# Performance work log

Hardware: AMD Instinct MI355X
Metric: run time of the kernel (lower is better)

Reference implementation:

```python
import jax, jax.numpy as jnp
import numpy as np
from jax import lax

sg = lax.stop_gradient

# (kernel, stride, pad, pool_k, pool_s) for the 7 conv blocks
CFG = [(16, 2, 7, 8, 4), (12, 2, 5, 4, 2), (9, 1, 4, 5, 2), (7, 1, 3, 4, 2),
       (5, 1, 2, 2, 2), (3, 1, 1, 2, 2), (3, 1, 1, 2, 2)]
W_SHAPES = [(8, 1, 16), (12, 8, 12), (32, 12, 9), (64, 32, 7),
            (64, 64, 5), (64, 64, 3), (72, 64, 3)]
CH = [8, 12, 32, 64, 64, 64, 72]


def bin_act(x):
    # forward: sign(x); backward: clipped-quadratic surrogate (STE)
    s = jnp.sign(x)
    le = (x < -1.0).astype(x.dtype)
    ri = (x >= 1.0).astype(x.dtype)
    cl = ((x >= -1.0) & (x < 0.0)).astype(x.dtype)
    cr = ((x >= 0.0) & (x < 1.0)).astype(x.dtype)
    out = cl * (2.0 + x) * x + cr * (2.0 - x) * x + ri - le
    return sg(s) + out - sg(out)


def bin_wei(w, axes):
    # forward: scale * sign(w) with scale = mean|w| (detached); backward through tanh (STE)
    scale = sg(jnp.mean(jnp.abs(w), axis=axes, keepdims=True))
    t = jnp.tanh(w)
    return sg(scale * jnp.sign(w)) + t - sg(t)


def conv1d(x, w, stride, pad):
    return lax.conv_general_dilated(x, w, (stride,), [(pad, pad)],
                                    dimension_numbers=('NCH', 'OIH', 'NCH'))


def maxpool1d(x, k, s):
    return lax.reduce_window(x, -jnp.inf, lax.max, (1, 1, k), (1, 1, s), 'VALID')


def batchnorm1d(x, gamma, beta, eps=1e-5):
    # training-mode BN: batch statistics over (N, L), biased variance
    m = jnp.mean(x, axis=(0, 2), keepdims=True)
    v = jnp.mean((x - m) ** 2, axis=(0, 2), keepdims=True)
    return gamma[None, :, None] * (x - m) / jnp.sqrt(v + eps) + beta[None, :, None]


def _forward(x, ws, gs, bs, wfc):
    for w, g, b, (k, s, p, pk, ps) in zip(ws, gs, bs, CFG):
        x = conv1d(x, bin_wei(w, (1, 2)), s, p)
        x = maxpool1d(x, pk, ps)
        x = batchnorm1d(x, g, b)
        x = bin_act(x)
    x = x.reshape(x.shape[0], -1)                 # [B, 72*3]
    return x @ bin_wei(wfc, (1,)).T               # [B, classCount]


def setup_inputs() -> dict:
    key = jax.random.key(0)
    ks = jax.random.split(key, 9)
    inp = {'x': jax.random.normal(ks[0], (2048, 1, 3600), dtype=jnp.float32)}
    for i, shp in enumerate(W_SHAPES):
        inp[f'w{i+1}'] = jax.random.uniform(ks[i + 1], shp, dtype=jnp.float32) * 0.32
        inp[f'g{i+1}'] = jnp.ones((CH[i],), jnp.float32)
        inp[f'b{i+1}'] = jnp.zeros((CH[i],), jnp.float32)
    inp['wfc'] = jax.random.uniform(ks[8], (5, 216), dtype=jnp.float32) * 0.32
    return inp


def reference(x, w1, w2, w3, w4, w5, w6, w7,
              g1, g2, g3, g4, g5, g6, g7,
              b1, b2, b3, b4, b5, b6, b7, wfc):
    ws = [w1, w2, w3, w4, w5, w6, w7]
    gs = [g1, g2, g3, g4, g5, g6, g7]
    bs = [b1, b2, b3, b4, b5, b6, b7]
    return _forward(x, ws, gs, bs, wfc)
```

## Files before the change

kernel.cpp:

```cpp
#include <hip/hip_runtime.h>
#include <math.h>
#include <stdint.h>

#define NBATCH 2048
#define NSLOT 32

struct Args {
    const float* x;
    const float* W[7];
    const float* G[7];
    const float* Bt[7];
    const float* WFC;
    float* out;
    float* bufA;
    float* bufB;
    double* stats;
    float* wsc;
    uint32_t* wmb;
};

__device__ __forceinline__ float signf(float v) {
    return (v > 0.f) ? 1.f : ((v < 0.f) ? -1.f : 0.f);
}

__global__ __launch_bounds__(256) void k_setup(Args a) {
    const int blk = blockIdx.x, tid = threadIdx.x;
    for (int i = blk * 256 + tid; i < NSLOT * 632; i += 391 * 256) a.stats[i] = 0.0;

    if (blk < 321 && tid < 64) {
        const int cum[9] = {0,8,20,52,116,180,244,316,321};
        const int per[8] = {16,96,108,224,320,192,192,216};
        const float* wsrc[8] = {a.W[0],a.W[1],a.W[2],a.W[3],a.W[4],a.W[5],a.W[6],a.WFC};
        int o = blk, L = 0;
        while (L < 7 && o >= cum[L + 1]) ++L;
        const int oo = o - cum[L], p = per[L];
        const float* wo = wsrc[L] + (size_t)oo * p;
        float s = 0.f;
        for (int i = tid; i < p; i += 64) s += fabsf(wo[i]);
        #pragma unroll
        for (int off = 32; off; off >>= 1) s += __shfl_down(s, off);
        if (tid == 0) a.wsc[o] = s / (float)p;
    }

    const int gid = (blk - 384) * 256 + tid;
    if (blk >= 384 && gid >= 0 && gid < 1608) {
        const int cum[7]  = {0,144,432,880,1200,1392,1608};
        const int cin[6]  = {8,12,32,64,64,64};
        const int kk[6]   = {12,9,7,5,3,3};
        const int wpp[6]  = {1,1,1,2,2,2};
        const int woff[6] = {0,144,432,880,1520,1904};
        const float* wsrc[6] = {a.W[1],a.W[2],a.W[3],a.W[4],a.W[5],a.W[6]};
        int L = 0;
        while (L < 5 && gid >= cum[L + 1]) ++L;
        const int idx = gid - cum[L];
        const int K = kk[L], CIN = cin[L], WPP = wpp[L];
        const int o = idx / K, k = idx - o * K;
        const float* w = wsrc[L];
        uint32_t m0 = 0, m1 = 0;
        for (int c = 0; c < CIN; ++c) {
            const float v = w[((size_t)o * CIN + c) * K + k];
            const uint32_t bit = (v < 0.f) ? 1u : 0u;
            int bp = c;
            if (CIN == 64) bp = 16 * (c & 3) + (c >> 2);
            else if (CIN == 32) bp = 8 * (c & 3) + (c >> 2);
            if (bp < 32) m0 |= bit << bp; else m1 |= bit << (bp - 32);
        }
        uint32_t* dst = a.wmb + woff[L] + (size_t)idx * WPP;
        dst[0] = m0;
        if (WPP == 2) dst[1] = m1;
    }
}

__global__ __launch_bounds__(256) void k_conv1(Args a) {
    __shared__ float wgs[128];
    __shared__ double sred[16];
    const int n = blockIdx.x, tid = threadIdx.x, l = tid & 63;
    if (tid < 128) wgs[tid] = signf(a.W[0][tid]);
    if (tid < 16)  sred[tid] = 0.0;
    __syncthreads();
    const int r = tid;
    const float* xn = a.x + (size_t)n * 3600;
    float m0[8], m1[8];
    #pragma unroll
    for (int ch = 0; ch < 8; ++ch) { m0[ch] = 0.f; m1[ch] = 0.f; }
    if (r < 225) {
        float f[40];
        const int g0 = 16 * r - 8;
        #pragma unroll
        for (int b = 0; b < 10; ++b) {
            const int gg = g0 + 4 * b;
            if (gg >= 0 && gg <= 3596) {
                const float4 v = *(const float4*)(xn + gg);
                f[4*b] = v.x; f[4*b+1] = v.y; f[4*b+2] = v.z; f[4*b+3] = v.w;
            } else {
                f[4*b] = 0.f; f[4*b+1] = 0.f; f[4*b+2] = 0.f; f[4*b+3] = 0.f;
            }
        }
        #pragma unroll
        for (int ch = 0; ch < 8; ++ch) {
            float acc[12];
            #pragma unroll
            for (int j = 0; j < 12; ++j) acc[j] = 0.f;
            #pragma unroll
            for (int k = 0; k < 16; ++k) {
                const float wk = wgs[ch * 16 + k];
                #pragma unroll
                for (int j = 0; j < 12; ++j)
                    acc[j] = fmaf(f[2*j + 1 + k], wk, acc[j]);
            }
            const float lo  = fmaxf(fmaxf(acc[0], acc[1]), fmaxf(acc[2], acc[3]));
            const float mid = fmaxf(fmaxf(acc[4], acc[5]), fmaxf(acc[6], acc[7]));
            const float hi  = fmaxf(fmaxf(acc[8], acc[9]), fmaxf(acc[10], acc[11]));
            const float sc = a.wsc[ch];
            m0[ch] = fmaxf(lo, mid) * sc;
            m1[ch] = (r < 224) ? fmaxf(mid, hi) * sc : 0.f;
        }
        float* on = a.bufA + ((size_t)n * 449 + 2 * r) * 8;
        *(float4*)(on + 0) = make_float4(m0[0], m0[1], m0[2], m0[3]);
        *(float4*)(on + 4) = make_float4(m0[4], m0[5], m0[6], m0[7]);
        if (r < 224) {
            *(float4*)(on + 8)  = make_float4(m1[0], m1[1], m1[2], m1[3]);
            *(float4*)(on + 12) = make_float4(m1[4], m1[5], m1[6], m1[7]);
        }
    }
    #pragma unroll
    for (int ch = 0; ch < 8; ++ch) {
        double sS = (double)m0[ch] + (double)m1[ch];
        double s2 = (double)m0[ch] * m0[ch] + (double)m1[ch] * m1[ch];
        #pragma unroll
        for (int off = 32; off; off >>= 1) {
            sS += __shfl_down(sS, off);
            s2 += __shfl_down(s2, off);
        }
        if (l == 0) {
            atomicAdd(&sred[ch], sS);
            atomicAdd(&sred[8 + ch], s2);
        }
    }
    __syncthreads();
    if (tid < 16) {
        double* so = a.stats + (size_t)(n & (NSLOT - 1)) * 16;
        atomicAdd(&so[tid], sred[tid]);
    }
}

template <int CIN, int LIN, int O, int K, int STRIDE, int PAD,
          int PK, int PS, int LP, int WPP, int LPB, bool SF64>
__device__ __forceinline__ void bin_body(
    const float* __restrict__ xprev, const uint32_t* __restrict__ wm,
    const float* __restrict__ wsc, const float* __restrict__ wsc_prev,
    const double* __restrict__ stats_in,
    const float* __restrict__ gamma, const float* __restrict__ beta,
    const double cntInv, float* __restrict__ out, double* __restrict__ stats_out)
{
    constexpr int OL    = (O < 64) ? O : 64;
    constexpr int PO    = 64 / OL;
    constexpr int SPAN  = (PK - 1) * STRIDE + K;
    constexpr int SHIFT = (WPP == 1) ? (PAD & 1) : 0;
    constexpr int QSPAN = 4 * LPB * PS * STRIDE + SPAN + 2;
    constexpr int XM64A = (WPP == 2) ? QSPAN : ((QSPAN + 3) / 2 + 1);
    constexpr int F     = 2 * CIN;
    constexpr int FW    = (F > 64) ? 128 : 64;

    __shared__ uint64_t xmbuf[XM64A];
    __shared__ long long foldU[4][FW];
    __shared__ int sS[4][O], sS2[4][O];

    const int tid = threadIdx.x;
    const int wv  = tid >> 6;
    const int l   = tid & 63;
    uint32_t* xm32 = (uint32_t*)xmbuf;
    uint64_t* xm64 = xmbuf;

    const int n    = blockIdx.x;
    const int lp0b = blockIdx.y * (4 * LPB);
    const int lp1b = (lp0b + 4 * LPB < LP) ? lp0b + 4 * LPB : LP;
    const int q0raw = lp0b * PS * STRIDE - PAD;
    const int q0 = (q0raw > 0) ? q0raw : 0;
    const int q1raw = (lp1b - 1) * PS * STRIDE - PAD + SPAN;
    const int q1 = (q1raw < LIN) ? q1raw : LIN;
    const int S0 = (WPP == 1) ? ((q0 + SHIFT) & 1) : 0;
    const int xbase = q0 - S0;

    const int lp0 = lp0b + wv * LPB;
    const int lp1 = (lp0 + LPB < lp1b) ? lp0 + LPB : lp1b;

    const float* xn = xprev + (size_t)n * LIN * CIN;

    {
        const long long* stI = (const long long*)stats_in;
        long long pa = 0, pb_ = 0;
        double da = 0.0;
        #pragma unroll
        for (int s8 = 0; s8 < 8; ++s8) {
            const int s = (wv << 3) + s8;
            if constexpr (SF64) {
                if (l < F) da += stats_in[s * F + l];
            } else {
                if (l < ((F < 64) ? F : 64)) pa += stI[s * F + l];
                if constexpr (F > 64) { if (l < F - 64) pb_ += stI[s * F + 64 + l]; }
            }
        }
        if constexpr (SF64) foldU[wv][l] = __double_as_longlong(da);
        else {
            foldU[wv][l] = pa;
            if constexpr (F > 64) foldU[wv][64 + l] = pb_;
        }
    }
    __syncthreads();
    float aA = 0.f, aB = 0.f;
    {
        double t0 = 0.0, t1 = 0.0;
        if constexpr (SF64) {
            double tot = 0.0;
            #pragma unroll
            for (int w = 0; w < 4; ++w) tot += __longlong_as_double(foldU[w][l]);
            t0 = tot;
            t1 = __shfl(tot, CIN + l);
        } else if constexpr (F > 64) {
            long long a0 = 0, a1 = 0;
            #pragma unroll
            for (int w = 0; w < 4; ++w) { a0 += foldU[w][l]; a1 += foldU[w][64 + l]; }
            t0 = (double)a0; t1 = (double)a1;
        } else {
            long long a0 = 0;
            #pragma unroll
            for (int w = 0; w < 4; ++w) a0 += foldU[w][l];
            const double tot = (double)a0;
            t0 = tot;
            t1 = __shfl(tot, CIN + l);
        }
        if (l < CIN) {
            double mean, E2;
            if constexpr (SF64) { mean = t0 * cntInv; E2 = t1 * cntInv; }
            else {
                const double w = (double)wsc_prev[l];
                mean = w * t0 * cntInv; E2 = w * w * t1 * cntInv;
            }
            const double var = E2 - mean * mean;
            const double inv = 1.0 / sqrt(var + 1e-5);
            const double av  = (double)gamma[l] * inv;
            aA = (float)av;
            aB = (float)((double)beta[l] - mean * av);
        }
    }

    if constexpr (CIN == 64) {
        const int sub = l & 15, grp = l >> 4;
        const float a0 = __shfl(aA, 4*sub),     b0 = __shfl(aB, 4*sub);
        const float a1 = __shfl(aA, 4*sub + 1), b1 = __shfl(aB, 4*sub + 1);
        const float a2 = __shfl(aA, 4*sub + 2), b2 = __shfl(aB, 4*sub + 2);
        const float a3 = __shfl(aA, 4*sub + 3), b3 = __shfl(aB, 4*sub + 3);
        for (int pb = q0 + wv * 4; pb < q1; pb += 16) {
            const int pos = pb + grp;
            const bool valid = pos < q1;
            const float4 v = *(const float4*)(xn + (size_t)(valid ? pos : q0) * 64 + 4*sub);
            const unsigned long long bal0 = __ballot(valid && (fmaf(a0, v.x, b0) < 0.f));
            const unsigned long long bal1 = __ballot(valid && (fmaf(a1, v.y, b1) < 0.f));
            const unsigned long long bal2 = __ballot(valid && (fmaf(a2, v.z, b2) < 0.f));
            const unsigned long long bal3 = __ballot(valid && (fmaf(a3, v.w, b3) < 0.f));
            if (l < 4 && pb + l < q1) {
                const uint64_t m = ((bal0 >> (16*l)) & 0xFFFFull)
                                 | (((bal1 >> (16*l)) & 0xFFFFull) << 16)
                                 | (((bal2 >> (16*l)) & 0xFFFFull) << 32)
                                 | (((bal3 >> (16*l)) & 0xFFFFull) << 48);
                xm64[pb + l - xbase] = m;
            }
        }
    } else if constexpr (CIN == 32) {
        const int sub = l & 7, grp = l >> 3;
        const float a0 = __shfl(aA, 4*sub),     b0 = __shfl(aB, 4*sub);
        const float a1 = __shfl(aA, 4*sub + 1), b1 = __shfl(aB, 4*sub + 1);
        const float a2 = __shfl(aA, 4*sub + 2), b2 = __shfl(aB, 4*sub + 2);
        const float a3 = __shfl(aA, 4*sub + 3), b3 = __shfl(aB, 4*sub + 3);
        for (int pb = q0 + wv * 8; pb < q1; pb += 32) {
            const int pos = pb + grp;
            const bool valid = pos < q1;
            const float4 v = *(const float4*)(xn + (size_t)(valid ? pos : q0) * 32 + 4*sub);
            const unsigned long long bal0 = __ballot(valid && (fmaf(a0, v.x, b0) < 0.f));
            const unsigned long long bal1 = __ballot(valid && (fmaf(a1, v.y, b1) < 0.f));
            const unsigned long long bal2 = __ballot(valid && (fmaf(a2, v.z, b2) < 0.f));
            const unsigned long long bal3 = __ballot(valid && (fmaf(a3, v.w, b3) < 0.f));
            if (l < 8 && pb + l < q1) {
                const uint32_t m = (uint32_t)((bal0 >> (8*l)) & 0xFFull)
                                 | ((uint32_t)((bal1 >> (8*l)) & 0xFFull) << 8)
                                 | ((uint32_t)((bal2 >> (8*l)) & 0xFFull) << 16)
                                 | ((uint32_t)((bal3 >> (8*l)) & 0xFFull) << 24);
                xm32[pb + l - xbase] = m;
            }
        }
    } else if constexpr (CIN == 8) {
        const int sub = l & 1, grp = l >> 1;
        const float a0 = __shfl(aA, 4*sub),     b0 = __shfl(aB, 4*sub);
        const float a1 = __shfl(aA, 4*sub + 1), b1 = __shfl(aB, 4*sub + 1);
        const float a2 = __shfl(aA, 4*sub + 2), b2 = __shfl(aB, 4*sub + 2);
        const float a3 = __shfl(aA, 4*sub + 3), b3 = __shfl(aB, 4*sub + 3);
        for (int pb = q0 + wv * 32; pb < q1; pb += 128) {
            const int pos = pb + grp;
            const bool valid = pos < q1;
            const float4 v = *(const float4*)(xn + (size_t)(valid ? pos : q0) * 8 + 4*sub);
            const unsigned long long bal0 = __ballot(valid && (fmaf(a0, v.x, b0) < 0.f));
            const unsigned long long bal1 = __ballot(valid && (fmaf(a1, v.y, b1) < 0.f));
            const unsigned long long bal2 = __ballot(valid && (fmaf(a2, v.z, b2) < 0.f));
            const unsigned long long bal3 = __ballot(valid && (fmaf(a3, v.w, b3) < 0.f));
            if (l < 32 && pb + l < q1) {
                const uint32_t t0 = (uint32_t)((bal0 >> (2*l)) & 3ull);
                const uint32_t t1 = (uint32_t)((bal1 >> (2*l)) & 3ull);
                const uint32_t t2 = (uint32_t)((bal2 >> (2*l)) & 3ull);
                const uint32_t t3 = (uint32_t)((bal3 >> (2*l)) & 3ull);
                const uint32_t m = (t0 & 1) | ((t1 & 1) << 1) | ((t2 & 1) << 2) | ((t3 & 1) << 3)
                                 | ((t0 >> 1) << 4) | ((t1 >> 1) << 5) | ((t2 >> 1) << 6) | ((t3 >> 1) << 7);
                xm32[pb + l - xbase] = m;
            }
        }
    } else {
        constexpr int PPW = 64 / CIN;
        const int pw = l / CIN, c = l - pw * CIN;
        const float myA = __shfl(aA, c), myB = __shfl(aB, c);
        const bool lact = (pw < PPW);
        for (int pb = q0 + wv * PPW; pb < q1; pb += 4 * PPW) {
            const int pos = pb + pw;
            const bool act = lact && (pos < q1);
            float v = 0.f;
            if (act) v = fmaf(myA, xn[(size_t)pb * CIN + l], myB);
            const unsigned long long bal = __ballot(act && (v < 0.f));
            if (act && c == 0) {
                const uint32_t mk = (uint32_t)((bal >> (pw * CIN)) & ((1u << CIN) - 1));
                xm32[pos - xbase] = mk;
            }
        }
    }
    __syncthreads();

    float* on = out + (size_t)n * LP * O;

    if constexpr (WPP == 2) {
        const uint64_t* wmp = (const uint64_t*)wm;
        uint64_t wr[K];
        #pragma unroll
        for (int k = 0; k < K; ++k) wr[k] = wmp[l * K + k];
        uint64_t wr2[K];
        const int oo2 = 64 + ((O > 64 && l < O - 64) ? l : 0);
        if constexpr (O > 64) {
            #pragma unroll
            for (int k = 0; k < K; ++k) wr2[k] = wmp[oo2 * K + k];
        }
        const float myws  = wsc[l];
        const float myws2 = (O > 64 && l < O - 64) ? wsc[64 + l] : 0.f;
        int accS = 0, accS2 = 0, accSb = 0, accS2b = 0;

        for (int lp = lp0; lp < lp1; ++lp) {
            const int lo = lp * PS * STRIDE - PAD;
            int m = -1000000, m2 = -1000000;
            if (lo >= 0 && lo + SPAN <= LIN) {
                uint64_t tw[SPAN];
                #pragma unroll
                for (int t = 0; t < SPAN; ++t) tw[t] = xm64[lo - xbase + t];
                #pragma unroll
                for (int j = 0; j < PK; ++j) {
                    int p = 0;
                    #pragma unroll
                    for (int k = 0; k < K; ++k)
                        p += __popcll(tw[j * STRIDE + k] ^ wr[k]);
                    m = max(m, CIN * K - 2 * p);
                    if constexpr (O > 64) {
                        int p2 = 0;
                        #pragma unroll
                        for (int k = 0; k < K; ++k)
                            p2 += __popcll(tw[j * STRIDE + k] ^ wr2[k]);
                        m2 = max(m2, CIN * K - 2 * p2);
                    }
                }
            } else {
                #pragma unroll
                for (int j = 0; j < PK; ++j) {
                    const int base = lo + j * STRIDE;
                    int p = 0, nv = 0, p2 = 0;
                    #pragma unroll
                    for (int k = 0; k < K; ++k) {
                        const int q = base + k;
                        if (q >= 0 && q < LIN) {
                            ++nv;
                            const uint64_t xv = xm64[q - xbase];
                            p += __popcll(xv ^ wr[k]);
                            if constexpr (O > 64) p2 += __popcll(xv ^ wr2[k]);
                        }
                    }
                    m = max(m, CIN * nv - 2 * p);
                    if constexpr (O > 64) m2 = max(m2, CIN * nv - 2 * p2);
                }
            }
            on[lp * O + l] = (float)m * myws;
            accS += m; accS2 += m * m;
            if constexpr (O > 64) {
                if (l < O - 64) {
                    on[lp * O + 64 + l] = (float)m2 * myws2;
                    accSb += m2; accS2b += m2 * m2;
                }
            }
        }
        sS[wv][l] = accS; sS2[wv][l] = accS2;
        if constexpr (O > 64) {
            if (l < O - 64) { sS[wv][64 + l] = accSb; sS2[wv][64 + l] = accS2b; }
        }
    } else {
        const int po = l / OL, oo = l - po * OL;
        const bool cact = (po < PO);
        const float myws = cact ? wsc[oo] : 0.f;
        uint32_t wr[K];
        #pragma unroll
        for (int k = 0; k < K; ++k) wr[k] = wm[(cact ? oo : 0) * K + k];
        int accS = 0, accS2 = 0;

        constexpr int PAIRS = (SPAN + 1) / 2;
        for (int lp = lp0 + po; lp < lp1; lp += PO) {
            const int lo = lp * PS * STRIDE - PAD;
            int m = -1000000;
            if (lo >= 0 && lo + SPAN <= LIN) {
                uint32_t tw[PAIRS * 2];
                const int e0 = (lo - xbase) >> 1;
                #pragma unroll
                for (int i = 0; i < PAIRS; ++i) {
                    const uint64_t u = xm64[e0 + i];
                    tw[2 * i]     = (uint32_t)u;
                    tw[2 * i + 1] = (uint32_t)(u >> 32);
                }
                #pragma unroll
                for (int j = 0; j < PK; ++j) {
                    int p = 0;
                    #pragma unroll
                    for (int k = 0; k < K; ++k)
                        p += __popc(tw[j * STRIDE + k] ^ wr[k]);
                    m = max(m, CIN * K - 2 * p);
                }
            } else {
                #pragma unroll
                for (int j = 0; j < PK; ++j) {
                    const int base = lo + j * STRIDE;
                    int p = 0, nv = 0;
                    #pragma unroll
                    for (int k = 0; k < K; ++k) {
                        const int q = base + k;
                        if (q >= 0 && q < LIN) { ++nv; p += __popc(xm32[q - xbase] ^ wr[k]); }
                    }
                    m = max(m, CIN * nv - 2 * p);
                }
            }
            if (cact) {
                on[lp * O + oo] = (float)m * myws;
                accS += m; accS2 += m * m;
            }
        }
        int t = accS, t2 = accS2;
        #pragma unroll
        for (int g = 1; g < PO; ++g) {
            t  += __shfl(accS,  l + g * OL);
            t2 += __shfl(accS2, l + g * OL);
        }
        if (l < OL) { sS[wv][l] = t; sS2[wv][l] = t2; }
    }
    __syncthreads();

    unsigned long long* soU =
        (unsigned long long*)stats_out + (size_t)(n & (NSLOT - 1)) * 2 * O;
    for (int t = tid; t < 2 * O; t += 256) {
        int tot;
        if (t < O) tot = sS[0][t] + sS[1][t] + sS[2][t] + sS[3][t];
        else { const int f = t - O; tot = sS2[0][f] + sS2[1][f] + sS2[2][f] + sS2[3][f]; }
        atomicAdd(&soU[t], (unsigned long long)(long long)tot);
    }
}

#define BIN_PARAMS \
    const float* __restrict__ xprev, const uint32_t* __restrict__ wm, \
    const float* __restrict__ wsc, const float* __restrict__ wsc_prev, \
    const double* __restrict__ stats_in, \
    const float* __restrict__ gamma, const float* __restrict__ beta, \
    const double cntInv, float* __restrict__ out, double* __restrict__ stats_out
#define BIN_ARGS xprev, wm, wsc, wsc_prev, stats_in, gamma, beta, cntInv, out, stats_out

__global__ __launch_bounds__(256) void k_bin2(BIN_PARAMS) { bin_body< 8,449,12,12,2,5,4,2,111,1,14,true >(BIN_ARGS); }
__global__ __launch_bounds__(256) void k_bin3(BIN_PARAMS) { bin_body<12,111,32, 9,1,4,5,2, 54,1,14,false>(BIN_ARGS); }
__global__ __launch_bounds__(256) void k_bin4(BIN_PARAMS) { bin_body<32, 54,64, 7,1,3,4,2, 26,1, 7,false>(BIN_ARGS); }
__global__ __launch_bounds__(256) void k_bin5(BIN_PARAMS) { bin_body<64, 26,64, 5,1,2,2,2, 13,2, 4,false>(BIN_ARGS); }
__global__ __launch_bounds__(256) void k_bin6(BIN_PARAMS) { bin_body<64, 13,64, 3,1,1,2,2,  6,2, 2,false>(BIN_ARGS); }
__global__ __launch_bounds__(256) void k_bin7(BIN_PARAMS) { bin_body<64,  6,72, 3,1,1,2,2,  3,2, 1,false>(BIN_ARGS); }

__global__ __launch_bounds__(256) void k_fc(Args a) {
    const int n = blockIdx.x * 4 + (int)(threadIdx.x >> 6);
    const int l = (int)(threadIdx.x & 63);
    const long long* st = (const long long*)(a.stats + 15616);
    long long s = 0, s2 = 0, sb = 0, s2b = 0;
    #pragma unroll 4
    for (int sl = 0; sl < NSLOT; ++sl) {
        s  += st[sl * 144 + l];
        s2 += st[sl * 144 + 72 + l];
        if (l < 8) {
            sb  += st[sl * 144 + 64 + l];
            s2b += st[sl * 144 + 72 + 64 + l];
        }
    }
    float aA0, aB0, aA1 = 0.f, aB1 = 0.f;
    {
        const double w = (double)a.wsc[244 + l];
        const double mean = w * (double)s / 6144.0;
        const double E2   = w * w * (double)s2 / 6144.0;
        const double var  = E2 - mean * mean;
        const double inv  = 1.0 / sqrt(var + 1e-5);
        const double aa   = (double)a.G[6][l] * inv;
        aA0 = (float)aa; aB0 = (float)((double)a.Bt[6][l] - mean * aa);
    }
    if (l < 8) {
        const double w = (double)a.wsc[244 + 64 + l];
        const double mean = w * (double)sb / 6144.0;
        const double E2   = w * w * (double)s2b / 6144.0;
        const double var  = E2 - mean * mean;
        const double inv  = 1.0 / sqrt(var + 1e-5);
        const double aa   = (double)a.G[6][64 + l] * inv;
        aA1 = (float)aa; aB1 = (float)((double)a.Bt[6][64 + l] - mean * aa);
    }
    const float* p7 = a.bufA + (size_t)n * 216;
    float acc[5] = {0.f, 0.f, 0.f, 0.f, 0.f};
    #pragma unroll
    for (int j = 0; j < 4; ++j) {
        const int i = l + 64 * j;
        const int ic = (i < 216) ? i : 215;
        const int c = ic / 3, lp = ic - 3 * c;
        float aa = __shfl(aA0, c);
        float bb = __shfl(aB0, c);
        const float aaH = __shfl(aA1, c - 64);
        const float bbH = __shfl(aB1, c - 64);
        if (c >= 64) { aa = aaH; bb = bbH; }
        if (i < 216) {
            const float av = signf(fmaf(aa, p7[lp * 72 + c], bb));
            #pragma unroll
            for (int o = 0; o < 5; ++o)
                acc[o] += av * signf(a.WFC[o * 216 + i]);
        }
    }
    #pragma unroll
    for (int o = 0; o < 5; ++o) {
        float v = acc[o];
        #pragma unroll
        for (int off = 32; off; off >>= 1) v += __shfl_down(v, off);
        if (l == 0) a.out[(size_t)n * 5 + o] = v * a.wsc[316 + o];
    }
}

extern "C" void kernel_launch(void* const* d_in, const int* in_sizes, int n_in,
                              void* d_out, int out_size, void* d_ws, size_t ws_size,
                              hipStream_t stream) {
    Args a;
    a.x = (const float*)d_in[0];
    for (int i = 0; i < 7; ++i) {
        a.W[i]  = (const float*)d_in[1 + 3 * i];
        a.G[i]  = (const float*)d_in[2 + 3 * i];
        a.Bt[i] = (const float*)d_in[3 + 3 * i];
    }
    a.WFC = (const float*)d_in[22];
    a.out = (float*)d_out;

    char* ws = (char*)d_ws;
    a.bufA  = (float*)ws;
    a.bufB  = (float*)(ws + 29425664);
    a.stats = (double*)(ws + 43057152);
    a.wsc   = (float*)(ws + 43218944);
    a.wmb   = (uint32_t*)d_out;

    k_setup<<<391, 256, 0, stream>>>(a);
    k_conv1<<<NBATCH, 256, 0, stream>>>(a);
    k_bin2<<<dim3(NBATCH, 2), 256, 0, stream>>>(
        a.bufA, a.wmb + 0, a.wsc + 8, a.wsc, a.stats + 0, a.G[0], a.Bt[0],
        1.0/919552.0, a.bufB, a.stats + 512);
    k_bin3<<<dim3(NBATCH, 1), 256, 0, stream>>>(
        a.bufB, a.wmb + 144, a.wsc + 20, a.wsc + 8, a.stats + 512, a.G[1], a.Bt[1],
        1.0/227328.0, a.bufA, a.stats + 1280);
    k_bin4<<<dim3(NBATCH, 1), 256, 0, stream>>>(
        a.bufA, a.wmb + 432, a.wsc + 52, a.wsc + 20, a.stats + 1280, a.G[2], a.Bt[2],
        1.0/110592.0, a.bufB, a.stats + 3328);
    k_bin5<<<dim3(NBATCH, 1), 256, 0, stream>>>(
        a.bufB, a.wmb + 880, a.wsc + 116, a.wsc + 52, a.stats + 3328, a.G[3], a.Bt[3],
        1.0/53248.0, a.bufA, a.stats + 7424);
    k_bin6<<<dim3(NBATCH, 1), 256, 0, stream>>>(
        a.bufA, a.wmb + 1520, a.wsc + 180, a.wsc + 116, a.stats + 7424, a.G[4], a.Bt[4],
        1.0/26624.0, a.bufB, a.stats + 11520);
    k_bin7<<<dim3(NBATCH, 1), 256, 0, stream>>>(
        a.bufB, a.wmb + 1904, a.wsc + 244, a.wsc + 180, a.stats + 11520, a.G[5], a.Bt[5],
        1.0/12288.0, a.bufA, a.stats + 15616);
    k_fc<<<NBATCH / 4, 256, 0, stream>>>(a);
}
```

Baseline: 272.6 us.

## Fuse binary layers and FC into one persistent kernel with grid barriers

Replaces the six per-layer binary-conv launches and the FC launch with a single persistent kernel of 1024 blocks. The blocks loop over samples and separate layers with a hierarchical atomic grid barrier. The goal is to remove kernel-launch gaps and tail drain between the small later layers. The risks are barrier spin cost, reduced parallelism for the large layer 2 (1024 blocks instead of 4096), and a guard-timeout exit that could break correctness if not all blocks are co-resident.

```diff
diff --git a/kernel.cpp b/kernel.cpp
--- a/kernel.cpp
+++ b/kernel.cpp
@@ -4,6 +4,7 @@
 
 #define NBATCH 2048
 #define NSLOT 32
+#define NB 1024
 
 struct Args {
     const float* x;
@@ -17,6 +18,7 @@
     double* stats;
     float* wsc;
     uint32_t* wmb;
+    uint32_t* bar;
 };
 
 __device__ __forceinline__ float signf(float v) {
@@ -26,6 +28,7 @@
 __global__ __launch_bounds__(256) void k_setup(Args a) {
     const int blk = blockIdx.x, tid = threadIdx.x;
     for (int i = blk * 256 + tid; i < NSLOT * 632; i += 391 * 256) a.stats[i] = 0.0;
+    if (blk == 0 && tid < 34) a.bar[tid] = 0u;
 
     if (blk < 321 && tid < 64) {
         const int cum[9] = {0,8,20,52,116,180,244,316,321};
@@ -144,9 +147,30 @@
     }
 }
 
+__device__ __forceinline__ void gridbar(uint32_t* bar, int p) {
+    __syncthreads();
+    if (threadIdx.x == 0) {
+        __threadfence();
+        const uint32_t tgt = 32u * (uint32_t)(p + 1);
+        uint32_t* sub = bar + 1 + (blockIdx.x & 31);
+        if (__hip_atomic_fetch_add(sub, 1u, __ATOMIC_RELAXED, __HIP_MEMORY_SCOPE_AGENT) == tgt - 1u) {
+            if (__hip_atomic_fetch_add(bar, 1u, __ATOMIC_RELAXED, __HIP_MEMORY_SCOPE_AGENT) == tgt - 1u) {
+                __hip_atomic_store(bar + 33, (uint32_t)(p + 1), __ATOMIC_RELAXED, __HIP_MEMORY_SCOPE_AGENT);
+            }
+        }
+        int guard = 0;
+        while (__hip_atomic_load(bar + 33, __ATOMIC_RELAXED, __HIP_MEMORY_SCOPE_AGENT) < (uint32_t)(p + 1)) {
+            __builtin_amdgcn_s_sleep(8);
+            if (++guard > 50000) break;
+        }
+        __threadfence();
+    }
+    __syncthreads();
+}
+
 template <int CIN, int LIN, int O, int K, int STRIDE, int PAD,
-          int PK, int PS, int LP, int WPP, int LPB, bool SF64>
-__device__ __forceinline__ void bin_body(
+          int PK, int PS, int LP, int WPP, int LPB, bool SF64, int NY>
+__device__ __forceinline__ void bin_layer(
     const float* __restrict__ xprev, const uint32_t* __restrict__ wm,
     const float* __restrict__ wsc, const float* __restrict__ wsc_prev,
     const double* __restrict__ stats_in,
@@ -172,21 +196,6 @@
     uint32_t* xm32 = (uint32_t*)xmbuf;
     uint64_t* xm64 = xmbuf;
 
-    const int n    = blockIdx.x;
-    const int lp0b = blockIdx.y * (4 * LPB);
-    const int lp1b = (lp0b + 4 * LPB < LP) ? lp0b + 4 * LPB : LP;
-    const int q0raw = lp0b * PS * STRIDE - PAD;
-    const int q0 = (q0raw > 0) ? q0raw : 0;
-    const int q1raw = (lp1b - 1) * PS * STRIDE - PAD + SPAN;
-    const int q1 = (q1raw < LIN) ? q1raw : LIN;
-    const int S0 = (WPP == 1) ? ((q0 + SHIFT) & 1) : 0;
-    const int xbase = q0 - S0;
-
-    const int lp0 = lp0b + wv * LPB;
-    const int lp1 = (lp0 + LPB < lp1b) ? lp0 + LPB : lp1b;
-
-    const float* xn = xprev + (size_t)n * LIN * CIN;
-
     {
         const long long* stI = (const long long*)stats_in;
         long long pa = 0, pb_ = 0;
@@ -244,251 +253,255 @@
             aB = (float)((double)beta[l] - mean * av);
         }
     }
-
-    if constexpr (CIN == 64) {
-        const int sub = l & 15, grp = l >> 4;
-        const float a0 = __shfl(aA, 4*sub),     b0 = __shfl(aB, 4*sub);
-        const float a1 = __shfl(aA, 4*sub + 1), b1 = __shfl(aB, 4*sub + 1);
-        const float a2 = __shfl(aA, 4*sub + 2), b2 = __shfl(aB, 4*sub + 2);
-        const float a3 = __shfl(aA, 4*sub + 3), b3 = __shfl(aB, 4*sub + 3);
-        for (int pb = q0 + wv * 4; pb < q1; pb += 16) {
-            const int pos = pb + grp;
-            const bool valid = pos < q1;
-            const float4 v = *(const float4*)(xn + (size_t)(valid ? pos : q0) * 64 + 4*sub);
-            const unsigned long long bal0 = __ballot(valid && (fmaf(a0, v.x, b0) < 0.f));
-            const unsigned long long bal1 = __ballot(valid && (fmaf(a1, v.y, b1) < 0.f));
-            const unsigned long long bal2 = __ballot(valid && (fmaf(a2, v.z, b2) < 0.f));
-            const unsigned long long bal3 = __ballot(valid && (fmaf(a3, v.w, b3) < 0.f));
-            if (l < 4 && pb + l < q1) {
-                const uint64_t m = ((bal0 >> (16*l)) & 0xFFFFull)
-                                 | (((bal1 >> (16*l)) & 0xFFFFull) << 16)
-                                 | (((bal2 >> (16*l)) & 0xFFFFull) << 32)
-                                 | (((bal3 >> (16*l)) & 0xFFFFull) << 48);
-                xm64[pb + l - xbase] = m;
-            }
-        }
-    } else if constexpr (CIN == 32) {
-        const int sub = l & 7, grp = l >> 3;
-        const float a0 = __shfl(aA, 4*sub),     b0 = __shfl(aB, 4*sub);
-        const float a1 = __shfl(aA, 4*sub + 1), b1 = __shfl(aB, 4*sub + 1);
-        const float a2 = __shfl(aA, 4*sub + 2), b2 = __shfl(aB, 4*sub + 2);
-        const float a3 = __shfl(aA, 4*sub + 3), b3 = __shfl(aB, 4*sub + 3);
-        for (int pb = q0 + wv * 8; pb < q1; pb += 32) {
-            const int pos = pb + grp;
-            const bool valid = pos < q1;
-            const float4 v = *(const float4*)(xn + (size_t)(valid ? pos : q0) * 32 + 4*sub);
-            const unsigned long long bal0 = __ballot(valid && (fmaf(a0, v.x, b0) < 0.f));
-            const unsigned long long bal1 = __ballot(valid && (fmaf(a1, v.y, b1) < 0.f));
-            const unsigned long long bal2 = __ballot(valid && (fmaf(a2, v.z, b2) < 0.f));
-            const unsigned long long bal3 = __ballot(valid && (fmaf(a3, v.w, b3) < 0.f));
-            if (l < 8 && pb + l < q1) {
-                const uint32_t m = (uint32_t)((bal0 >> (8*l)) & 0xFFull)
-                                 | ((uint32_t)((bal1 >> (8*l)) & 0xFFull) << 8)
-                                 | ((uint32_t)((bal2 >> (8*l)) & 0xFFull) << 16)
-                                 | ((uint32_t)((bal3 >> (8*l)) & 0xFFull) << 24);
-                xm32[pb + l - xbase] = m;
-            }
-        }
-    } else if constexpr (CIN == 8) {
-        const int sub = l & 1, grp = l >> 1;
-        const float a0 = __shfl(aA, 4*sub),     b0 = __shfl(aB, 4*sub);
-        const float a1 = __shfl(aA, 4*sub + 1), b1 = __shfl(aB, 4*sub + 1);
-        const float a2 = __shfl(aA, 4*sub + 2), b2 = __shfl(aB, 4*sub + 2);
-        const float a3 = __shfl(aA, 4*sub + 3), b3 = __shfl(aB, 4*sub + 3);
-        for (int pb = q0 + wv * 32; pb < q1; pb += 128) {
-            const int pos = pb + grp;
-            const bool valid = pos < q1;
-            const float4 v = *(const float4*)(xn + (size_t)(valid ? pos : q0) * 8 + 4*sub);
-            const unsigned long long bal0 = __ballot(valid && (fmaf(a0, v.x, b0) < 0.f));
-            const unsigned long long bal1 = __ballot(valid && (fmaf(a1, v.y, b1) < 0.f));
-            const unsigned long long bal2 = __ballot(valid && (fmaf(a2, v.z, b2) < 0.f));
-            const unsigned long long bal3 = __ballot(valid && (fmaf(a3, v.w, b3) < 0.f));
-            if (l < 32 && pb + l < q1) {
-                const uint32_t t0 = (uint32_t)((bal0 >> (2*l)) & 3ull);
-                const uint32_t t1 = (uint32_t)((bal1 >> (2*l)) & 3ull);
-                const uint32_t t2 = (uint32_t)((bal2 >> (2*l)) & 3ull);
-                const uint32_t t3 = (uint32_t)((bal3 >> (2*l)) & 3ull);
-                const uint32_t m = (t0 & 1) | ((t1 & 1) << 1) | ((t2 & 1) << 2) | ((t3 & 1) << 3)
-                                 | ((t0 >> 1) << 4) | ((t1 >> 1) << 5) | ((t2 >> 1) << 6) | ((t3 >> 1) << 7);
-                xm32[pb + l - xbase] = m;
-            }
-        }
-    } else {
-        constexpr int PPW = 64 / CIN;
-        const int pw = l / CIN, c = l - pw * CIN;
-        const float myA = __shfl(aA, c), myB = __shfl(aB, c);
-        const bool lact = (pw < PPW);
-        for (int pb = q0 + wv * PPW; pb < q1; pb += 4 * PPW) {
-            const int pos = pb + pw;
-            const bool act = lact && (pos < q1);
-            float v = 0.f;
-            if (act) v = fmaf(myA, xn[(size_t)pb * CIN + l], myB);
-            const unsigned long long bal = __ballot(act && (v < 0.f));
-            if (act && c == 0) {
-                const uint32_t mk = (uint32_t)((bal >> (pw * CIN)) & ((1u << CIN) - 1));
-                xm32[pos - xbase] = mk;
-            }
-        }
-    }
     __syncthreads();
 
-    float* on = out + (size_t)n * LP * O;
-
-    if constexpr (WPP == 2) {
-        const uint64_t* wmp = (const uint64_t*)wm;
-        uint64_t wr[K];
-        #pragma unroll
-        for (int k = 0; k < K; ++k) wr[k] = wmp[l * K + k];
-        uint64_t wr2[K];
-        const int oo2 = 64 + ((O > 64 && l < O - 64) ? l : 0);
-        if constexpr (O > 64) {
-            #pragma unroll
-            for (int k = 0; k < K; ++k) wr2[k] = wmp[oo2 * K + k];
-        }
-        const float myws  = wsc[l];
-        const float myws2 = (O > 64 && l < O - 64) ? wsc[64 + l] : 0.f;
-        int accS = 0, accS2 = 0, accSb = 0, accS2b = 0;
-
-        for (int lp = lp0; lp < lp1; ++lp) {
-            const int lo = lp * PS * STRIDE - PAD;
-            int m = -1000000, m2 = -1000000;
-            if (lo >= 0 && lo + SPAN <= LIN) {
-                uint64_t tw[SPAN];
+    for (int u = blockIdx.x; u < NBATCH * NY; u += NB) {
+        const int n  = (NY == 2) ? (u >> 1) : u;
+        const int yb = (NY == 2) ? (u & 1) : 0;
+        const int lp0b = yb * (4 * LPB);
+        const int lp1b = (lp0b + 4 * LPB < LP) ? lp0b + 4 * LPB : LP;
+        const int q0raw = lp0b * PS * STRIDE - PAD;
+        const int q0 = (q0raw > 0) ? q0raw : 0;
+        const int q1raw = (lp1b - 1) * PS * STRIDE - PAD + SPAN;
+        const int q1 = (q1raw < LIN) ? q1raw : LIN;
+        const int S0 = (WPP == 1) ? ((q0 + SHIFT) & 1) : 0;
+        const int xbase = q0 - S0;
+        const int lp0 = lp0b + wv * LPB;
+        const int lp1 = (lp0 + LPB < lp1b) ? lp0 + LPB : lp1b;
+        const float* xn = xprev + (size_t)n * LIN * CIN;
+
+        if constexpr (CIN == 64) {
+            const int sub = l & 15, grp = l >> 4;
+            const float a0 = __shfl(aA, 4*sub),     b0 = __shfl(aB, 4*sub);
+            const float a1 = __shfl(aA, 4*sub + 1), b1 = __shfl(aB, 4*sub + 1);
+            const float a2 = __shfl(aA, 4*sub + 2), b2 = __shfl(aB, 4*sub + 2);
+            const float a3 = __shfl(aA, 4*sub + 3), b3 = __shfl(aB, 4*sub + 3);
+            for (int pb = q0 + wv * 4; pb < q1; pb += 16) {
+                const int pos = pb + grp;
+                const bool valid = pos < q1;
+                const float4 v = *(const float4*)(xn + (size_t)(valid ? pos : q0) * 64 + 4*sub);
+                const unsigned long long bal0 = __ballot(valid && (fmaf(a0, v.x, b0) < 0.f));
+                const unsigned long long bal1 = __ballot(valid && (fmaf(a1, v.y, b1) < 0.f));
+                const unsigned long long bal2 = __ballot(valid && (fmaf(a2, v.z, b2) < 0.f));
+                const unsigned long long bal3 = __ballot(valid && (fmaf(a3, v.w, b3) < 0.f));
+                if (l < 4 && pb + l < q1) {
+                    const uint64_t m = ((bal0 >> (16*l)) & 0xFFFFull)
+                                     | (((bal1 >> (16*l)) & 0xFFFFull) << 16)
+                                     | (((bal2 >> (16*l)) & 0xFFFFull) << 32)
+                                     | (((bal3 >> (16*l)) & 0xFFFFull) << 48);
+                    xm64[pb + l - xbase] = m;
+                }
+            }
+        } else if constexpr (CIN == 32) {
+            const int sub = l & 7, grp = l >> 3;
+            const float a0 = __shfl(aA, 4*sub),     b0 = __shfl(aB, 4*sub);
+            const float a1 = __shfl(aA, 4*sub + 1), b1 = __shfl(aB, 4*sub + 1);
+            const float a2 = __shfl(aA, 4*sub + 2), b2 = __shfl(aB, 4*sub + 2);
+            const float a3 = __shfl(aA, 4*sub + 3), b3 = __shfl(aB, 4*sub + 3);
+            for (int pb = q0 + wv * 8; pb < q1; pb += 32) {
+                const int pos = pb + grp;
+                const bool valid = pos < q1;
+                const float4 v = *(const float4*)(xn + (size_t)(valid ? pos : q0) * 32 + 4*sub);
+                const unsigned long long bal0 = __ballot(valid && (fmaf(a0, v.x, b0) < 0.f));
+                const unsigned long long bal1 = __ballot(valid && (fmaf(a1, v.y, b1) < 0.f));
+                const unsigned long long bal2 = __ballot(valid && (fmaf(a2, v.z, b2) < 0.f));
+                const unsigned long long bal3 = __ballot(valid && (fmaf(a3, v.w, b3) < 0.f));
+                if (l < 8 && pb + l < q1) {
+                    const uint32_t m = (uint32_t)((bal0 >> (8*l)) & 0xFFull)
+                                     | ((uint32_t)((bal1 >> (8*l)) & 0xFFull) << 8)
+                                     | ((uint32_t)((bal2 >> (8*l)) & 0xFFull) << 16)
+                                     | ((uint32_t)((bal3 >> (8*l)) & 0xFFull) << 24);
+                    xm32[pb + l - xbase] = m;
+                }
+            }
+        } else if constexpr (CIN == 8) {
+            const int sub = l & 1, grp = l >> 1;
+            const float a0 = __shfl(aA, 4*sub),     b0 = __shfl(aB, 4*sub);
+            const float a1 = __shfl(aA, 4*sub + 1), b1 = __shfl(aB, 4*sub + 1);
+            const float a2 = __shfl(aA, 4*sub + 2), b2 = __shfl(aB, 4*sub + 2);
+            const float a3 = __shfl(aA, 4*sub + 3), b3 = __shfl(aB, 4*sub + 3);
+            for (int pb = q0 + wv * 32; pb < q1; pb += 128) {
+                const int pos = pb + grp;
+                const bool valid = pos < q1;
+                const float4 v = *(const float4*)(xn + (size_t)(valid ? pos : q0) * 8 + 4*sub);
+                const unsigned long long bal0 = __ballot(valid && (fmaf(a0, v.x, b0) < 0.f));
+                const unsigned long long bal1 = __ballot(valid && (fmaf(a1, v.y, b1) < 0.f));
+                const unsigned long long bal2 = __ballot(valid && (fmaf(a2, v.z, b2) < 0.f));
+                const unsigned long long bal3 = __ballot(valid && (fmaf(a3, v.w, b3) < 0.f));
+                if (l < 32 && pb + l < q1) {
+                    const uint32_t t0 = (uint32_t)((bal0 >> (2*l)) & 3ull);
+                    const uint32_t t1 = (uint32_t)((bal1 >> (2*l)) & 3ull);
+                    const uint32_t t2 = (uint32_t)((bal2 >> (2*l)) & 3ull);
+                    const uint32_t t3 = (uint32_t)((bal3 >> (2*l)) & 3ull);
+                    const uint32_t m = (t0 & 1) | ((t1 & 1) << 1) | ((t2 & 1) << 2) | ((t3 & 1) << 3)
+                                     | ((t0 >> 1) << 4) | ((t1 >> 1) << 5) | ((t2 >> 1) << 6) | ((t3 >> 1) << 7);
+                    xm32[pb + l - xbase] = m;
+                }
+            }
+        } else {
+            constexpr int PPW = 64 / CIN;
+            const int pw = l / CIN, c = l - pw * CIN;
+            const float myA = __shfl(aA, c), myB = __shfl(aB, c);
+            const bool lact = (pw < PPW);
+            for (int pb = q0 + wv * PPW; pb < q1; pb += 4 * PPW) {
+                const int pos = pb + pw;
+                const bool act = lact && (pos < q1);
+                float v = 0.f;
+                if (act) v = fmaf(myA, xn[(size_t)pb * CIN + l], myB);
+                const unsigned long long bal = __ballot(act && (v < 0.f));
+                if (act && c == 0) {
+                    const uint32_t mk = (uint32_t)((bal >> (pw * CIN)) & ((1u << CIN) - 1));
+                    xm32[pos - xbase] = mk;
+                }
+            }
+        }
+        __syncthreads();
+
+        float* on = out + (size_t)n * LP * O;
+
+        if constexpr (WPP == 2) {
+            const uint64_t* wmp = (const uint64_t*)wm;
+            uint64_t wr[K];
+            #pragma unroll
+            for (int k = 0; k < K; ++k) wr[k] = wmp[l * K + k];
+            uint64_t wr2[K];
+            const int oo2 = 64 + ((O > 64 && l < O - 64) ? l : 0);
+            if constexpr (O > 64) {
                 #pragma unroll
-                for (int t = 0; t < SPAN; ++t) tw[t] = xm64[lo - xbase + t];
-                #pragma unroll
-                for (int j = 0; j < PK; ++j) {
-                    int p = 0;
+                for (int k = 0; k < K; ++k) wr2[k] = wmp[oo2 * K + k];
+            }
+            const float myws  = wsc[l];
+            const float myws2 = (O > 64 && l < O - 64) ? wsc[64 + l] : 0.f;
+            int accS = 0, accS2 = 0, accSb = 0, accS2b = 0;
+
+            for (int lp = lp0; lp < lp1; ++lp) {
+                const int lo = lp * PS * STRIDE - PAD;
+                int m = -1000000, m2 = -1000000;
+                if (lo >= 0 && lo + SPAN <= LIN) {
+                    uint64_t tw[SPAN];
                     #pragma unroll
-                    for (int k = 0; k < K; ++k)
-                        p += __popcll(tw[j * STRIDE + k] ^ wr[k]);
-                    m = max(m, CIN * K - 2 * p);
-                    if constexpr (O > 64) {
-                        int p2 = 0;
+                    for (int t = 0; t < SPAN; ++t) tw[t] = xm64[lo - xbase + t];
+                    #pragma unroll
+                    for (int j = 0; j < PK; ++j) {
+                        int p = 0;
                         #pragma unroll
                         for (int k = 0; k < K; ++k)
-                            p2 += __popcll(tw[j * STRIDE + k] ^ wr2[k]);
-                        m2 = max(m2, CIN * K - 2 * p2);
-                    }
-                }
-            } else {
-                #pragma unroll
-                for (int j = 0; j < PK; ++j) {
-                    const int base = lo + j * STRIDE;
-                    int p = 0, nv = 0, p2 = 0;
-                    #pragma unroll
-                    for (int k = 0; k < K; ++k) {
-                        const int q = base + k;
-                        if (q >= 0 && q < LIN) {
-                            ++nv;
-                            const uint64_t xv = xm64[q - xbase];
-                            p += __popcll(xv ^ wr[k]);
-                            if constexpr (O > 64) p2 += __popcll(xv ^ wr2[k]);
+                            p += __popcll(tw[j * STRIDE + k] ^ wr[k]);
+                        m = max(m, CIN * K - 2 * p);
+                        if constexpr (O > 64) {
+                            int p2 = 0;
+                            #pragma unroll
+                            for (int k = 0; k < K; ++k)
+                                p2 += __popcll(tw[j * STRIDE + k] ^ wr2[k]);
+                            m2 = max(m2, CIN * K - 2 * p2);
                         }
                     }
-                    m = max(m, CIN * nv - 2 * p);
-                    if constexpr (O > 64) m2 = max(m2, CIN * nv - 2 * p2);
-                }
-            }
-            on[lp * O + l] = (float)m * myws;
-            accS += m; accS2 += m * m;
+                } else {
+                    #pragma unroll
+                    for (int j = 0; j < PK; ++j) {
+                        const int base = lo + j * STRIDE;
+                        int p = 0, nv = 0, p2 = 0;
+                        #pragma unroll
+                        for (int k = 0; k < K; ++k) {
+                            const int q = base + k;
+                            if (q >= 0 && q < LIN) {
+                                ++nv;
+                                const uint64_t xv = xm64[q - xbase];
+                                p += __popcll(xv ^ wr[k]);
+                                if constexpr (O > 64) p2 += __popcll(xv ^ wr2[k]);
+                            }
+                        }
+                        m = max(m, CIN * nv - 2 * p);
+                        if constexpr (O > 64) m2 = max(m2, CIN * nv - 2 * p2);
+                    }
+                }
+                on[lp * O + l] = (float)m * myws;
+                accS += m; accS2 += m * m;
+                if constexpr (O > 64) {
+                    if (l < O - 64) {
+                        on[lp * O + 64 + l] = (float)m2 * myws2;
+                        accSb += m2; accS2b += m2 * m2;
+                    }
+                }
+            }
+            sS[wv][l] = accS; sS2[wv][l] = accS2;
             if constexpr (O > 64) {
-                if (l < O - 64) {
-                    on[lp * O + 64 + l] = (float)m2 * myws2;
-                    accSb += m2; accS2b += m2 * m2;
-                }
-            }
-        }
-        sS[wv][l] = accS; sS2[wv][l] = accS2;
-        if constexpr (O > 64) {
-            if (l < O - 64) { sS[wv][64 + l] = accSb; sS2[wv][64 + l] = accS2b; }
-        }
-    } else {
-        const int po = l / OL, oo = l - po * OL;
-        const bool cact = (po < PO);
-        const float myws = cact ? wsc[oo] : 0.f;
-        uint32_t wr[K];
-        #pragma unroll
-        for (int k = 0; k < K; ++k) wr[k] = wm[(cact ? oo : 0) * K + k];
-        int accS = 0, accS2 = 0;
-
-        constexpr int PAIRS = (SPAN + 1) / 2;
-        for (int lp = lp0 + po; lp < lp1; lp += PO) {
-            const int lo = lp * PS * STRIDE - PAD;
-            int m = -1000000;
-            if (lo >= 0 && lo + SPAN <= LIN) {
-                uint32_t tw[PAIRS * 2];
-                const int e0 = (lo - xbase) >> 1;
-                #pragma unroll
-                for (int i = 0; i < PAIRS; ++i) {
-                    const uint64_t u = xm64[e0 + i];
-                    tw[2 * i]     = (uint32_t)u;
-                    tw[2 * i + 1] = (uint32_t)(u >> 32);
-                }
-                #pragma unroll
-                for (int j = 0; j < PK; ++j) {
-                    int p = 0;
+                if (l < O - 64) { sS[wv][64 + l] = accSb; sS2[wv][64 + l] = accS2b; }
+            }
+        } else {
+            const int po = l / OL, oo = l - po * OL;
+            const bool cact = (po < PO);
+            const float myws = cact ? wsc[oo] : 0.f;
+            uint32_t wr[K];
+            #pragma unroll
+            for (int k = 0; k < K; ++k) wr[k] = wm[(cact ? oo : 0) * K + k];
+            int accS = 0, accS2 = 0;
+
+            constexpr int PAIRS = (SPAN + 1) / 2;
+            for (int lp = lp0 + po; lp < lp1; lp += PO) {
+                const int lo = lp * PS * STRIDE - PAD;
+                int m = -1000000;
+                if (lo >= 0 && lo + SPAN <= LIN) {
+                    uint32_t tw[PAIRS * 2];
+                    const int e0 = (lo - xbase) >> 1;
                     #pragma unroll
-                    for (int k = 0; k < K; ++k)
-                        p += __popc(tw[j * STRIDE + k] ^ wr[k]);
-                    m = max(m, CIN * K - 2 * p);
-                }
-            } else {
-                #pragma unroll
-                for (int j = 0; j < PK; ++j) {
-                    const int base = lo + j * STRIDE;
-                    int p = 0, nv = 0;
+                    for (int i = 0; i < PAIRS; ++i) {
+                        const uint64_t u64v = xm64[e0 + i];
+                        tw[2 * i]     = (uint32_t)u64v;
+                        tw[2 * i + 1] = (uint32_t)(u64v >> 32);
+                    }
                     #pragma unroll
-                    for (int k = 0; k < K; ++k) {
-                        const int q = base + k;
-                        if (q >= 0 && q < LIN) { ++nv; p += __popc(xm32[q - xbase] ^ wr[k]); }
+                    for (int j = 0; j < PK; ++j) {
+                        int p = 0;
+                        #pragma unroll
+                        for (int k = 0; k < K; ++k)
+                            p += __popc(tw[j * STRIDE + k] ^ wr[k]);
+                        m = max(m, CIN * K - 2 * p);
                     }
-                    m = max(m, CIN * nv - 2 * p);
-                }
-            }
-            if (cact) {
-                on[lp * O + oo] = (float)m * myws;
-                accS += m; accS2 += m * m;
-            }
-        }
-        int t = accS, t2 = accS2;
-        #pragma unroll
-        for (int g = 1; g < PO; ++g) {
-            t  += __shfl(accS,  l + g * OL);
-            t2 += __shfl(accS2, l + g * OL);
-        }
-        if (l < OL) { sS[wv][l] = t; sS2[wv][l] = t2; }
-    }
-    __syncthreads();
-
-    unsigned long long* soU =
-        (unsigned long long*)stats_out + (size_t)(n & (NSLOT - 1)) * 2 * O;
-    for (int t = tid; t < 2 * O; t += 256) {
-        int tot;
-        if (t < O) tot = sS[0][t] + sS[1][t] + sS[2][t] + sS[3][t];
-        else { const int f = t - O; tot = sS2[0][f] + sS2[1][f] + sS2[2][f] + sS2[3][f]; }
-        atomicAdd(&soU[t], (unsigned long long)(long long)tot);
-    }
-}
-
-#define BIN_PARAMS \
-    const float* __restrict__ xprev, const uint32_t* __restrict__ wm, \
-    const float* __restrict__ wsc, const float* __restrict__ wsc_prev, \
-    const double* __restrict__ stats_in, \
-    const float* __restrict__ gamma, const float* __restrict__ beta, \
-    const double cntInv, float* __restrict__ out, double* __restrict__ stats_out
-#define BIN_ARGS xprev, wm, wsc, wsc_prev, stats_in, gamma, beta, cntInv, out, stats_out
-
-__global__ __launch_bounds__(256) void k_bin2(BIN_PARAMS) { bin_body< 8,449,12,12,2,5,4,2,111,1,14,true >(BIN_ARGS); }
-__global__ __launch_bounds__(256) void k_bin3(BIN_PARAMS) { bin_body<12,111,32, 9,1,4,5,2, 54,1,14,false>(BIN_ARGS); }
-__global__ __launch_bounds__(256) void k_bin4(BIN_PARAMS) { bin_body<32, 54,64, 7,1,3,4,2, 26,1, 7,false>(BIN_ARGS); }
-__global__ __launch_bounds__(256) void k_bin5(BIN_PARAMS) { bin_body<64, 26,64, 5,1,2,2,2, 13,2, 4,false>(BIN_ARGS); }
-__global__ __launch_bounds__(256) void k_bin6(BIN_PARAMS) { bin_body<64, 13,64, 3,1,1,2,2,  6,2, 2,false>(BIN_ARGS); }
-__global__ __launch_bounds__(256) void k_bin7(BIN_PARAMS) { bin_body<64,  6,72, 3,1,1,2,2,  3,2, 1,false>(BIN_ARGS); }
-
-__global__ __launch_bounds__(256) void k_fc(Args a) {
-    const int n = blockIdx.x * 4 + (int)(threadIdx.x >> 6);
-    const int l = (int)(threadIdx.x & 63);
+                } else {
+                    #pragma unroll
+                    for (int j = 0; j < PK; ++j) {
+                        const int base = lo + j * STRIDE;
+                        int p = 0, nv = 0;
+                        #pragma unroll
+                        for (int k = 0; k < K; ++k) {
+                            const int q = base + k;
+                            if (q >= 0 && q < LIN) { ++nv; p += __popc(xm32[q - xbase] ^ wr[k]); }
+                        }
+                        m = max(m, CIN * nv - 2 * p);
+                    }
+                }
+                if (cact) {
+                    on[lp * O + oo] = (float)m * myws;
+                    accS += m; accS2 += m * m;
+                }
+            }
+            int t = accS, t2 = accS2;
+            #pragma unroll
+            for (int g = 1; g < PO; ++g) {
+                t  += __shfl(accS,  l + g * OL);
+                t2 += __shfl(accS2, l + g * OL);
+            }
+            if (l < OL) { sS[wv][l] = t; sS2[wv][l] = t2; }
+        }
+        __syncthreads();
+
+        unsigned long long* soU =
+            (unsigned long long*)stats_out + (size_t)(n & (NSLOT - 1)) * 2 * O;
+        for (int t = tid; t < 2 * O; t += 256) {
+            int tot;
+            if (t < O) tot = sS[0][t] + sS[1][t] + sS[2][t] + sS[3][t];
+            else { const int f = t - O; tot = sS2[0][f] + sS2[1][f] + sS2[2][f] + sS2[3][f]; }
+            atomicAdd(&soU[t], (unsigned long long)(long long)tot);
+        }
+        __syncthreads();
+    }
+}
+
+__device__ __forceinline__ void fc_phase(const Args& a) {
+    const int wv = (int)(threadIdx.x >> 6), l = (int)(threadIdx.x & 63);
+    const int n = blockIdx.x * 4 + wv;
+    if (n >= NBATCH) return;
     const long long* st = (const long long*)(a.stats + 15616);
     long long s = 0, s2 = 0, sb = 0, s2b = 0;
     #pragma unroll 4
@@ -547,6 +560,34 @@
     }
 }
 
+__global__ __launch_bounds__(256, 4) void k_fused(Args a) {
+    bin_layer< 8,449,12,12,2,5,4,2,111,1,14,true ,2>(
+        a.bufA, a.wmb + 0, a.wsc + 8, a.wsc, a.stats + 0, a.G[0], a.Bt[0],
+        1.0/919552.0, a.bufB, a.stats + 512);
+    gridbar(a.bar, 0);
+    bin_layer<12,111,32, 9,1,4,5,2, 54,1,14,false,1>(
+        a.bufB, a.wmb + 144, a.wsc + 20, a.wsc + 8, a.stats + 512, a.G[1], a.Bt[1],
+        1.0/227328.0, a.bufA, a.stats + 1280);
+    gridbar(a.bar, 1);
+    bin_layer<32, 54,64, 7,1,3,4,2, 26,1, 7,false,1>(
+        a.bufA, a.wmb + 432, a.wsc + 52, a.wsc + 20, a.stats + 1280, a.G[2], a.Bt[2],
+        1.0/110592.0, a.bufB, a.stats + 3328);
+    gridbar(a.bar, 2);
+    bin_layer<64, 26,64, 5,1,2,2,2, 13,2, 4,false,1>(
+        a.bufB, a.wmb + 880, a.wsc + 116, a.wsc + 52, a.stats + 3328, a.G[3], a.Bt[3],
+        1.0/53248.0, a.bufA, a.stats + 7424);
+    gridbar(a.bar, 3);
+    bin_layer<64, 13,64, 3,1,1,2,2,  6,2, 2,false,1>(
+        a.bufA, a.wmb + 1520, a.wsc + 180, a.wsc + 116, a.stats + 7424, a.G[4], a.Bt[4],
+        1.0/26624.0, a.bufB, a.stats + 11520);
+    gridbar(a.bar, 4);
+    bin_layer<64,  6,72, 3,1,1,2,2,  3,2, 1,false,1>(
+        a.bufB, a.wmb + 1904, a.wsc + 244, a.wsc + 180, a.stats + 11520, a.G[5], a.Bt[5],
+        1.0/12288.0, a.bufA, a.stats + 15616);
+    gridbar(a.bar, 5);
+    fc_phase(a);
+}
+
 extern "C" void kernel_launch(void* const* d_in, const int* in_sizes, int n_in,
                               void* d_out, int out_size, void* d_ws, size_t ws_size,
                               hipStream_t stream) {
@@ -565,27 +606,10 @@
     a.bufB  = (float*)(ws + 29425664);
     a.stats = (double*)(ws + 43057152);
     a.wsc   = (float*)(ws + 43218944);
+    a.bar   = (uint32_t*)(ws + 43220480);
     a.wmb   = (uint32_t*)d_out;
 
     k_setup<<<391, 256, 0, stream>>>(a);
     k_conv1<<<NBATCH, 256, 0, stream>>>(a);
-    k_bin2<<<dim3(NBATCH, 2), 256, 0, stream>>>(
-        a.bufA, a.wmb + 0, a.wsc + 8, a.wsc, a.stats + 0, a.G[0], a.Bt[0],
-        1.0/919552.0, a.bufB, a.stats + 512);
-    k_bin3<<<dim3(NBATCH, 1), 256, 0, stream>>>(
-        a.bufB, a.wmb + 144, a.wsc + 20, a.wsc + 8, a.stats + 512, a.G[1], a.Bt[1],
-        1.0/227328.0, a.bufA, a.stats + 1280);
-    k_bin4<<<dim3(NBATCH, 1), 256, 0, stream>>>(
-        a.bufA, a.wmb + 432, a.wsc + 52, a.wsc + 20, a.stats + 1280, a.G[2], a.Bt[2],
-        1.0/110592.0, a.bufB, a.stats + 3328);
-    k_bin5<<<dim3(NBATCH, 1), 256, 0, stream>>>(
-        a.bufB, a.wmb + 880, a.wsc + 116, a.wsc + 52, a.stats + 3328, a.G[3], a.Bt[3],
-        1.0/53248.0, a.bufA, a.stats + 7424);
-    k_bin6<<<dim3(NBATCH, 1), 256, 0, stream>>>(
-        a.bufA, a.wmb + 1520, a.wsc + 180, a.wsc + 116, a.stats + 7424, a.G[4], a.Bt[4],
-        1.0/26624.0, a.bufB, a.stats + 11520);
-    k_bin7<<<dim3(NBATCH, 1), 256, 0, stream>>>(
-        a.bufB, a.wmb + 1904, a.wsc + 244, a.wsc + 180, a.stats + 11520, a.G[5], a.Bt[5],
-        1.0/12288.0, a.bufA, a.stats + 15616);
-    k_fc<<<NBATCH / 4, 256, 0, stream>>>(a);
-}
+    k_fused<<<NB, 256, 0, stream>>>(a);
+}
```

Result: slower. 521.7 us (+91.4%).
